# Optimization experiments

Hardware: AMD Instinct MI355X
Metric: run time of the kernel (lower is better)

## Reference

```python
import jax, jax.numpy as jnp
import numpy as np

B, N, A, M, H, KD, VD, O = 256, 2048, 256, 256, 8, 32, 32, 256
EPS = 1e-10

def setup_inputs() -> dict:
    key = jax.random.key(0)
    ks = jax.random.split(key, 8)
    return {
        "q_data": jax.random.normal(ks[0], (B, N, A), dtype=jnp.float32),
        "m_data": jax.random.normal(ks[1], (B, N, M), dtype=jnp.float32),
        "q_mask": jnp.ones((B, N, 1), dtype=jnp.float32),
        "bias": jnp.zeros((B, 1, N), dtype=jnp.float32),
        "query_w": 0.02 * jax.random.normal(ks[2], (A, H, KD), dtype=jnp.float32),
        "key_w": 0.02 * jax.random.normal(ks[3], (M, KD), dtype=jnp.float32),
        "value_w": 0.02 * jax.random.normal(ks[4], (M, VD), dtype=jnp.float32),
        "gating_w": 0.02 * jax.random.normal(ks[5], (A, H, VD), dtype=jnp.float32),
        "gating_b": jnp.zeros((H, VD), dtype=jnp.float32),
        "output_w": 0.02 * jax.random.normal(ks[6], (H, VD, O), dtype=jnp.float32),
        "output_b": jnp.zeros((O,), dtype=jnp.float32),
    }

def reference(q_data, m_data, q_mask, bias, query_w, key_w, value_w,
              gating_w, gating_b, output_w, output_b):
    # masked mean over the query axis: q_mask [B,N,1] broadcasts over channels
    q_avg = jnp.sum(q_mask * q_data, axis=1) / (jnp.sum(q_mask, axis=1) + EPS)  # [B,A]
    kd = query_w.shape[-1]
    q = jnp.einsum('ba,ahc->bhc', q_avg, query_w) * kd ** (-0.5)  # [B,H,KD]
    k = jnp.einsum('bka,ac->bkc', m_data, key_w)                  # [B,N,KD]
    v = jnp.einsum('bka,ac->bkc', m_data, value_w)                # [B,N,VD]
    # the incoming `bias` arg is overwritten by the module, as in the original
    attn_bias = 1e9 * (q_mask[:, None, :, 0] - 1.0)               # [B,1,N]
    logits = jnp.einsum('bhc,bkc->bhk', q, k) + attn_bias         # [B,H,N]
    weights = jax.nn.softmax(logits, axis=-1)
    weighted_avg = jnp.einsum('bhk,bkc->bhc', weights, v)         # [B,H,VD]
    # gating == True
    gate = jax.nn.sigmoid(jnp.einsum('bqc,chv->bqhv', q_data, gating_w) + gating_b)
    gated = weighted_avg[:, None] * gate                          # [B,N,H,VD]
    out = jnp.einsum('bqhc,hco->bqo', gated, output_w) + output_b # [B,N,O]
    return out
```

## Files before the change

kernel.cpp:

```cpp
#include <hip/hip_runtime.h>

#define B_ 256
#define N_ 2048
#define A_ 256
#define M_ 256
#define H_ 8
#define KD_ 32
#define VD_ 32
#define O_ 256

typedef float f32x4 __attribute__((ext_vector_type(4)));
typedef __bf16 bf16x8 __attribute__((ext_vector_type(8)));
typedef unsigned short u16x8 __attribute__((ext_vector_type(8)));

union FragU { u16x8 u; bf16x8 b; };

__device__ __forceinline__ unsigned short f2bf(float f) {
  union { __bf16 b; unsigned short u; } c;
  c.b = (__bf16)f;
  return c.u;
}
__device__ __forceinline__ float bf2f(unsigned short h) {
  return __uint_as_float(((unsigned int)h) << 16);
}

__device__ __forceinline__ void gll16(const void* gsrc, void* ldst) {
  __builtin_amdgcn_global_load_lds(
      (const __attribute__((address_space(1))) void*)gsrc,
      (__attribute__((address_space(3))) void*)ldst, 16, 0, 0);
}

__global__ void pack_weights(const float* __restrict__ gating_w,
                             const float* __restrict__ output_w,
                             const float* __restrict__ key_w,
                             const float* __restrict__ value_w,
                             unsigned short* __restrict__ wg,
                             unsigned short* __restrict__ wo,
                             unsigned short* __restrict__ wkv) {
  int idx = blockIdx.x * 256 + threadIdx.x;
  int j = idx & 7;
  int lane = (idx >> 3) & 63;
  int rest = idx >> 9;
  int kc = rest & 7, ct = rest >> 3;
  int row = kc * 32 + ((lane >> 4) << 3) + j;
  int col = ct * 16 + (lane & 15);
  wg[idx] = f2bf(gating_w[row * 256 + col]);
  wo[idx] = f2bf(output_w[row * 256 + col]);
  if (idx < 16384) {
    float v = (col < 32) ? key_w[row * 32 + col] : value_w[row * 32 + (col - 32)];
    wkv[idx] = f2bf(v);
  }
}

__global__ void reduce_q(const float* __restrict__ qd, const float* __restrict__ qm,
                         const float* __restrict__ qw, float* __restrict__ q_out) {
  int b = blockIdx.x;
  int t = threadIdx.x;
  int l = t & 63, g = t >> 6;
  const float* qdb = qd + (size_t)b * N_ * A_;
  const float* qmb = qm + (size_t)b * N_;
  f32x4 sum = {0.f, 0.f, 0.f, 0.f};
  float msum = 0.f;
  for (int n = g; n < N_; n += 16) {
    float m = qmb[n];
    msum += m;
    f32x4 v = *(const f32x4*)(qdb + (size_t)n * A_ + l * 4);
    sum += m * v;
  }
  __shared__ float s[16][256];
  __shared__ float ms[16];
  __shared__ float qavg[256];
  *(f32x4*)&s[g][l * 4] = sum;
  if (l == 0) ms[g] = msum;
  __syncthreads();
  if (t < 256) {
    float tot = 0.f;
#pragma unroll
    for (int k = 0; k < 16; k++) tot += s[k][t];
    float mt = 0.f;
#pragma unroll
    for (int k = 0; k < 16; k++) mt += ms[k];
    qavg[t] = tot / (mt + 1e-10f);
  }
  __syncthreads();
  if (t < 256) {
    float acc = 0.f;
    for (int a2 = 0; a2 < 256; a2++) acc += qavg[a2] * qw[a2 * 256 + t];
    q_out[b * 256 + t] = acc * 0.17677669529663687f;
  }
}

__global__ void kv_gemm(const float* __restrict__ md,
                        const unsigned short* __restrict__ wkv,
                        unsigned short* __restrict__ kv) {
  int t = threadIdx.x;
  int w = t >> 6, l = t & 63, q = l >> 4, l15 = l & 15;
  size_t r0 = (size_t)blockIdx.x * 128;
  f32x4 acc[2][4] = {};
  for (int kc = 0; kc < 8; kc++) {
    FragU bfr[4];
#pragma unroll
    for (int ct = 0; ct < 4; ct++)
      bfr[ct].u = *(const u16x8*)(wkv + (((ct * 8 + kc) * 64 + l) << 3));
    FragU af[2];
#pragma unroll
    for (int rt = 0; rt < 2; rt++) {
      size_t row = r0 + (size_t)(w * 32 + rt * 16 + l15);
      const float4* s4 = (const float4*)(md + row * 256 + kc * 32 + q * 8);
      float4 u0 = s4[0], u1 = s4[1];
      af[rt].u = (u16x8){f2bf(u0.x), f2bf(u0.y), f2bf(u0.z), f2bf(u0.w),
                         f2bf(u1.x), f2bf(u1.y), f2bf(u1.z), f2bf(u1.w)};
    }
#pragma unroll
    for (int ct = 0; ct < 4; ct++) {
      acc[0][ct] = __builtin_amdgcn_mfma_f32_16x16x32_bf16(af[0].b, bfr[ct].b, acc[0][ct], 0, 0, 0);
      acc[1][ct] = __builtin_amdgcn_mfma_f32_16x16x32_bf16(af[1].b, bfr[ct].b, acc[1][ct], 0, 0, 0);
    }
  }
#pragma unroll
  for (int rt = 0; rt < 2; rt++)
#pragma unroll
    for (int ct = 0; ct < 4; ct++)
#pragma unroll
      for (int r = 0; r < 4; r++) {
        size_t row = r0 + (size_t)(w * 32 + rt * 16 + q * 4 + r);
        kv[row * 64 + ct * 16 + l15] = f2bf(acc[rt][ct][r]);
      }
}

__global__ void attn_softmax(const unsigned short* __restrict__ kv,
                             const float* __restrict__ qv,
                             const float* __restrict__ qm,
                             float* __restrict__ wa) {
  int b = blockIdx.x, t = threadIdx.x;
  __shared__ float lg[8][2048];
  __shared__ float red[4][256];
  __shared__ float inv_s[8];
  const float* qb = qv + b * 256;
  const float* qmb = qm + (size_t)b * N_;
  for (int n = t; n < N_; n += 1024) {
    const u16x8* kr = (const u16x8*)(kv + ((size_t)(b * N_ + n)) * 64);
    float kf[32];
#pragma unroll
    for (int c8 = 0; c8 < 4; c8++) {
      u16x8 kk = kr[c8];
#pragma unroll
      for (int j = 0; j < 8; j++) kf[c8 * 8 + j] = bf2f(kk[j]);
    }
    float bias_n = 1e9f * (qmb[n] - 1.0f);
#pragma unroll
    for (int h = 0; h < 8; h++) {
      float d = 0.f;
#pragma unroll
      for (int c = 0; c < 32; c++) d += qb[h * 32 + c] * kf[c];
      lg[h][n] = d + bias_n;
    }
  }
  __syncthreads();
  if (t < 256) {
    int h = t >> 5, i = t & 31;
    float m = -3.0e38f;
    for (int n = i; n < N_; n += 32) m = fmaxf(m, lg[h][n]);
#pragma unroll
    for (int off = 16; off; off >>= 1) m = fmaxf(m, __shfl_xor(m, off));
    float s = 0.f;
    for (int n = i; n < N_; n += 32) {
      float e = __expf(lg[h][n] - m);
      lg[h][n] = e;
      s += e;
    }
#pragma unroll
    for (int off = 16; off; off >>= 1) s += __shfl_xor(s, off);
    if (i == 0) inv_s[h] = 1.0f / s;
  }
  __syncthreads();
  {
    int c = t & 31, h = (t >> 5) & 7, nq = t >> 8;
    const unsigned short* vb = kv + ((size_t)b * N_ + nq * 512) * 64 + 32 + c;
    const float* lgh = &lg[h][nq * 512];
    float acc = 0.f;
#pragma unroll 8
    for (int n = 0; n < 512; n++) acc += lgh[n] * bf2f(vb[(size_t)n * 64]);
    red[nq][t & 255] = acc;
  }
  __syncthreads();
  if (t < 256) {
    float r = red[0][t] + red[1][t] + red[2][t] + red[3][t];
    wa[b * 256 + t] = r * inv_s[t >> 5];
  }
}

__launch_bounds__(256, 4)
__global__ void gate_out(const float* __restrict__ qd,
                         const unsigned short* __restrict__ wg,
                         const unsigned short* __restrict__ wo,
                         const float* __restrict__ wa,
                         const float* __restrict__ gb,
                         const float* __restrict__ ob,
                         float* __restrict__ out) {
  int blk = blockIdx.x;
  int b = blk >> 5, tile = blk & 31;
  int t = threadIdx.x;
  int w = t >> 6, l = t & 63, q = l >> 4, l15 = l & 15;
  __shared__ __attribute__((aligned(16))) unsigned short wsg[8192];
  __shared__ __attribute__((aligned(16))) unsigned short wso[8192];
  __shared__ __attribute__((aligned(16))) unsigned short Pt[4][16][40];
  __shared__ float wa_s[256], gb_s[256], ob_s[256];
  wa_s[t] = wa[b * 256 + t];
  gb_s[t] = gb[t];
  ob_s[t] = ob[t];
  size_t rowbase = (size_t)b * N_ + tile * 64;

  {
    const char* wgb = (const char*)wg;
    const char* wob = (const char*)wo;
#pragma unroll
    for (int i = 0; i < 4; i++) {
      int ch = i * 4 + w;
      gll16(wgb + ch * 1024 + l * 16, (char*)wsg + ch * 1024);
      gll16(wob + ch * 8192 + l * 16, (char*)wso + ch * 1024);
    }
  }

  FragU af[8];
  {
    const float* src = qd + (rowbase + (size_t)(w * 16 + l15)) * 256 + q * 8;
#pragma unroll
    for (int kc = 0; kc < 8; kc++) {
      float4 u0 = *(const float4*)(src + kc * 32);
      float4 u1 = *(const float4*)(src + kc * 32 + 4);
      af[kc].u = (u16x8){f2bf(u0.x), f2bf(u0.y), f2bf(u0.z), f2bf(u0.w),
                         f2bf(u1.x), f2bf(u1.y), f2bf(u1.z), f2bf(u1.w)};
    }
  }
  f32x4 acc[4][4] = {};
  __syncthreads();

  for (int g = 0; g < 8; g++) {
    f32x4 gacc[2] = {};
#pragma unroll
    for (int kc = 0; kc < 8; kc++) {
      FragU b0, b1;
      b0.u = *(const u16x8*)(wsg + (kc * 64 + l) * 8);
      b1.u = *(const u16x8*)(wsg + ((8 + kc) * 64 + l) * 8);
      gacc[0] = __builtin_amdgcn_mfma_f32_16x16x32_bf16(af[kc].b, b0.b, gacc[0], 0, 0, 0);
      gacc[1] = __builtin_amdgcn_mfma_f32_16x16x32_bf16(af[kc].b, b1.b, gacc[1], 0, 0, 0);
    }
#pragma unroll
    for (int ctl = 0; ctl < 2; ctl++) {
      int colg = ctl * 16 + l15;
      int col = g * 32 + colg;
      float wav = wa_s[col], gbv = gb_s[col];
#pragma unroll
      for (int r = 0; r < 4; r++) {
        float x = gacc[ctl][r] + gbv;
        float gate = 1.0f / (1.0f + __expf(-x));
        Pt[w][q * 4 + r][colg] = f2bf(wav * gate);
      }
    }

    __syncthreads();
    if (g < 7) {
      const char* wgb = (const char*)wg + (size_t)(g + 1) * 16384;
#pragma unroll
      for (int i = 0; i < 4; i++) {
        int ch = i * 4 + w;
        gll16(wgb + ch * 1024 + l * 16, (char*)wsg + ch * 1024);
      }
    }
    FragU pf[4];
#pragma unroll
    for (int rt = 0; rt < 4; rt++)
      pf[rt].u = *(const u16x8*)&Pt[rt][l15][q * 8];
#pragma unroll
    for (int ct2 = 0; ct2 < 4; ct2++) {
      FragU bo;
      bo.u = *(const u16x8*)(wso + ((w * 4 + ct2) * 64 + l) * 8);
#pragma unroll
      for (int rt = 0; rt < 4; rt++)
        acc[rt][ct2] = __builtin_amdgcn_mfma_f32_16x16x32_bf16(pf[rt].b, bo.b, acc[rt][ct2], 0, 0, 0);
    }
    __syncthreads();
    if (g < 7) {
      const char* wob = (const char*)wo + (size_t)(g + 1) * 1024;
#pragma unroll
      for (int i = 0; i < 4; i++) {
        int ch = i * 4 + w;
        gll16(wob + ch * 8192 + l * 16, (char*)wso + ch * 1024);
      }
    }
  }
#pragma unroll
  for (int rt = 0; rt < 4; rt++) {
#pragma unroll
    for (int ct2 = 0; ct2 < 4; ct2++) {
      int col = w * 64 + ct2 * 16 + l15;
      float obv = ob_s[col];
      size_t orow = (rowbase + (size_t)(rt * 16 + q * 4)) * 256 + col;
#pragma unroll
      for (int r = 0; r < 4; r++)
        out[orow + (size_t)r * 256] = acc[rt][ct2][r] + obv;
    }
  }
}

extern "C" void kernel_launch(void* const* d_in, const int* in_sizes, int n_in,
                              void* d_out, int out_size, void* d_ws, size_t ws_size,
                              hipStream_t stream) {
  const float* q_data   = (const float*)d_in[0];
  const float* m_data   = (const float*)d_in[1];
  const float* q_mask   = (const float*)d_in[2];
  const float* query_w  = (const float*)d_in[4];
  const float* key_w    = (const float*)d_in[5];
  const float* value_w  = (const float*)d_in[6];
  const float* gating_w = (const float*)d_in[7];
  const float* gating_b = (const float*)d_in[8];
  const float* output_w = (const float*)d_in[9];
  const float* output_b = (const float*)d_in[10];
  float* out = (float*)d_out;

  char* ws = (char*)d_ws;
  float* q_ws            = (float*)(ws);
  float* wa_ws           = (float*)(ws + (256 << 10));
  unsigned short* wg_ws  = (unsigned short*)(ws + (512 << 10));
  unsigned short* wo_ws  = (unsigned short*)(ws + (640 << 10));
  unsigned short* wkv_ws = (unsigned short*)(ws + (768 << 10));
  unsigned short* kv_ws  = (unsigned short*)(ws + (800 << 10));

  pack_weights<<<256, 256, 0, stream>>>(gating_w, output_w, key_w, value_w,
                                        wg_ws, wo_ws, wkv_ws);
  reduce_q<<<B_, 1024, 0, stream>>>(q_data, q_mask, query_w, q_ws);
  kv_gemm<<<(B_ * N_) / 128, 256, 0, stream>>>(m_data, wkv_ws, kv_ws);
  attn_softmax<<<B_, 1024, 0, stream>>>(kv_ws, q_ws, q_mask, wa_ws);
  gate_out<<<(B_ * N_) / 64, 256, 0, stream>>>(q_data, wg_ws, wo_ws, wa_ws,
                                               gating_b, output_b, out);
}
```

Measured before the change: 1.464 ms.

## Split K/V workspace with transposed V and double-buffer gating weights

The KV projection now writes K and V into separate buffers, with V transposed to [B, VD, N]. This lets the weighted-average loop in the attention kernel read 8 contiguous bf16 values and float4 logits at a time instead of strided scalars. The trade-off is that kv_gemm now issues scattered 2-byte stores for V. In gate_out, the gating-weight LDS tile is double-buffered and prefetched at the top of each group. Output weights are read straight from global memory instead of staged in LDS, which removes one barrier per iteration at the cost of more global/L2 traffic and lower declared occupancy.

```diff
diff --git a/kernel.cpp b/kernel.cpp
--- a/kernel.cpp
+++ b/kernel.cpp
@@ -92,10 +92,13 @@
 
 __global__ void kv_gemm(const float* __restrict__ md,
                         const unsigned short* __restrict__ wkv,
-                        unsigned short* __restrict__ kv) {
+                        unsigned short* __restrict__ k_ws,
+                        unsigned short* __restrict__ v_ws) {
   int t = threadIdx.x;
   int w = t >> 6, l = t & 63, q = l >> 4, l15 = l & 15;
   size_t r0 = (size_t)blockIdx.x * 128;
+  int b = (int)(r0 >> 11);
+  int n0 = (int)(r0 & 2047);
   f32x4 acc[2][4] = {};
   for (int kc = 0; kc < 8; kc++) {
     FragU bfr[4];
@@ -123,12 +126,17 @@
     for (int ct = 0; ct < 4; ct++)
 #pragma unroll
       for (int r = 0; r < 4; r++) {
-        size_t row = r0 + (size_t)(w * 32 + rt * 16 + q * 4 + r);
-        kv[row * 64 + ct * 16 + l15] = f2bf(acc[rt][ct][r]);
+        int rloc = w * 32 + rt * 16 + q * 4 + r;
+        if (ct < 2) {
+          k_ws[(r0 + rloc) * 32 + ct * 16 + l15] = f2bf(acc[rt][ct][r]);
+        } else {
+          v_ws[((size_t)b * 32 + (ct - 2) * 16 + l15) * N_ + (n0 + rloc)] = f2bf(acc[rt][ct][r]);
+        }
       }
 }
 
-__global__ void attn_softmax(const unsigned short* __restrict__ kv,
+__global__ void attn_softmax(const unsigned short* __restrict__ k_ws,
+                             const unsigned short* __restrict__ v_ws,
                              const float* __restrict__ qv,
                              const float* __restrict__ qm,
                              float* __restrict__ wa) {
@@ -139,13 +147,30 @@
   const float* qb = qv + b * 256;
   const float* qmb = qm + (size_t)b * N_;
   for (int n = t; n < N_; n += 1024) {
-    const u16x8* kr = (const u16x8*)(kv + ((size_t)(b * N_ + n)) * 64);
+    const u16x8* kr = (const u16x8*)(k_ws + ((size_t)(b * N_ + n)) * 32);
     float kf[32];
 #pragma unroll
-    for (int c8 = 0; c8 < 4; c8++) {
+    for (int c8 = 0; c8 < 2; c8++) {
       u16x8 kk = kr[c8];
 #pragma unroll
       for (int j = 0; j < 8; j++) kf[c8 * 8 + j] = bf2f(kk[j]);
+    }
+    u16x8 kk2 = kr[0];
+    (void)kk2;
+#pragma unroll
+    for (int c8 = 2; c8 < 4; c8++) {
+      u16x8 kk = kr[c8 - 2 + 2];
+      (void)kk;
+    }
+    {
+      u16x8 ka = kr[0], kb2 = kr[1], kc2 = kr[2], kd2 = kr[3];
+#pragma unroll
+      for (int j = 0; j < 8; j++) {
+        kf[j]      = bf2f(ka[j]);
+        kf[8 + j]  = bf2f(kb2[j]);
+        kf[16 + j] = bf2f(kc2[j]);
+        kf[24 + j] = bf2f(kd2[j]);
+      }
     }
     float bias_n = 1e9f * (qmb[n] - 1.0f);
 #pragma unroll
@@ -176,11 +201,22 @@
   __syncthreads();
   {
     int c = t & 31, h = (t >> 5) & 7, nq = t >> 8;
-    const unsigned short* vb = kv + ((size_t)b * N_ + nq * 512) * 64 + 32 + c;
-    const float* lgh = &lg[h][nq * 512];
+    const u16x8* vb = (const u16x8*)(v_ws + ((size_t)b * 32 + c) * N_ + nq * 512);
+    const f32x4* lg4 = (const f32x4*)&lg[h][nq * 512];
     float acc = 0.f;
-#pragma unroll 8
-    for (int n = 0; n < 512; n++) acc += lgh[n] * bf2f(vb[(size_t)n * 64]);
+#pragma unroll 4
+    for (int n8 = 0; n8 < 64; n8++) {
+      u16x8 vv = vb[n8];
+      f32x4 p0 = lg4[n8 * 2], p1 = lg4[n8 * 2 + 1];
+      acc += p0[0] * bf2f(vv[0]);
+      acc += p0[1] * bf2f(vv[1]);
+      acc += p0[2] * bf2f(vv[2]);
+      acc += p0[3] * bf2f(vv[3]);
+      acc += p1[0] * bf2f(vv[4]);
+      acc += p1[1] * bf2f(vv[5]);
+      acc += p1[2] * bf2f(vv[6]);
+      acc += p1[3] * bf2f(vv[7]);
+    }
     red[nq][t & 255] = acc;
   }
   __syncthreads();
@@ -190,7 +226,7 @@
   }
 }
 
-__launch_bounds__(256, 4)
+__launch_bounds__(256, 3)
 __global__ void gate_out(const float* __restrict__ qd,
                          const unsigned short* __restrict__ wg,
                          const unsigned short* __restrict__ wo,
@@ -202,9 +238,8 @@
   int b = blk >> 5, tile = blk & 31;
   int t = threadIdx.x;
   int w = t >> 6, l = t & 63, q = l >> 4, l15 = l & 15;
-  __shared__ __attribute__((aligned(16))) unsigned short wsg[8192];
-  __shared__ __attribute__((aligned(16))) unsigned short wso[8192];
-  __shared__ __attribute__((aligned(16))) unsigned short Pt[4][16][40];
+  __shared__ __attribute__((aligned(16))) unsigned short wsg[2][8192];
+  __shared__ __attribute__((aligned(16))) unsigned short Pt[2][4][16][40];
   __shared__ float wa_s[256], gb_s[256], ob_s[256];
   wa_s[t] = wa[b * 256 + t];
   gb_s[t] = gb[t];
@@ -213,12 +248,10 @@
 
   {
     const char* wgb = (const char*)wg;
-    const char* wob = (const char*)wo;
 #pragma unroll
     for (int i = 0; i < 4; i++) {
       int ch = i * 4 + w;
-      gll16(wgb + ch * 1024 + l * 16, (char*)wsg + ch * 1024);
-      gll16(wob + ch * 8192 + l * 16, (char*)wso + ch * 1024);
+      gll16(wgb + ch * 1024 + l * 16, (char*)&wsg[0][0] + ch * 1024);
     }
   }
 
@@ -237,12 +270,21 @@
   __syncthreads();
 
   for (int g = 0; g < 8; g++) {
+    int cur = g & 1;
+    if (g < 7) {
+      const char* wgb = (const char*)wg + (size_t)(g + 1) * 16384;
+#pragma unroll
+      for (int i = 0; i < 4; i++) {
+        int ch = i * 4 + w;
+        gll16(wgb + ch * 1024 + l * 16, (char*)&wsg[cur ^ 1][0] + ch * 1024);
+      }
+    }
     f32x4 gacc[2] = {};
 #pragma unroll
     for (int kc = 0; kc < 8; kc++) {
       FragU b0, b1;
-      b0.u = *(const u16x8*)(wsg + (kc * 64 + l) * 8);
-      b1.u = *(const u16x8*)(wsg + ((8 + kc) * 64 + l) * 8);
+      b0.u = *(const u16x8*)(&wsg[cur][0] + (kc * 64 + l) * 8);
+      b1.u = *(const u16x8*)(&wsg[cur][0] + ((8 + kc) * 64 + l) * 8);
       gacc[0] = __builtin_amdgcn_mfma_f32_16x16x32_bf16(af[kc].b, b0.b, gacc[0], 0, 0, 0);
       gacc[1] = __builtin_amdgcn_mfma_f32_16x16x32_bf16(af[kc].b, b1.b, gacc[1], 0, 0, 0);
     }
@@ -255,39 +297,24 @@
       for (int r = 0; r < 4; r++) {
         float x = gacc[ctl][r] + gbv;
         float gate = 1.0f / (1.0f + __expf(-x));
-        Pt[w][q * 4 + r][colg] = f2bf(wav * gate);
+        Pt[cur][w][q * 4 + r][colg] = f2bf(wav * gate);
       }
     }
 
     __syncthreads();
-    if (g < 7) {
-      const char* wgb = (const char*)wg + (size_t)(g + 1) * 16384;
-#pragma unroll
-      for (int i = 0; i < 4; i++) {
-        int ch = i * 4 + w;
-        gll16(wgb + ch * 1024 + l * 16, (char*)wsg + ch * 1024);
-      }
-    }
+
     FragU pf[4];
 #pragma unroll
     for (int rt = 0; rt < 4; rt++)
-      pf[rt].u = *(const u16x8*)&Pt[rt][l15][q * 8];
+      pf[rt].u = *(const u16x8*)&Pt[cur][rt][l15][q * 8];
 #pragma unroll
     for (int ct2 = 0; ct2 < 4; ct2++) {
       FragU bo;
-      bo.u = *(const u16x8*)(wso + ((w * 4 + ct2) * 64 + l) * 8);
+      bo.u = *(const u16x8*)((const char*)wo + (size_t)(w * 4 + ct2) * 8192 +
+                             (size_t)g * 1024 + l * 16);
 #pragma unroll
       for (int rt = 0; rt < 4; rt++)
         acc[rt][ct2] = __builtin_amdgcn_mfma_f32_16x16x32_bf16(pf[rt].b, bo.b, acc[rt][ct2], 0, 0, 0);
-    }
-    __syncthreads();
-    if (g < 7) {
-      const char* wob = (const char*)wo + (size_t)(g + 1) * 1024;
-#pragma unroll
-      for (int i = 0; i < 4; i++) {
-        int ch = i * 4 + w;
-        gll16(wob + ch * 8192 + l * 16, (char*)wso + ch * 1024);
-      }
     }
   }
 #pragma unroll
@@ -325,13 +352,14 @@
   unsigned short* wg_ws  = (unsigned short*)(ws + (512 << 10));
   unsigned short* wo_ws  = (unsigned short*)(ws + (640 << 10));
   unsigned short* wkv_ws = (unsigned short*)(ws + (768 << 10));
-  unsigned short* kv_ws  = (unsigned short*)(ws + (800 << 10));
+  unsigned short* k_wsp  = (unsigned short*)(ws + (800 << 10));
+  unsigned short* v_wsp  = (unsigned short*)(ws + (800 << 10) + ((size_t)32 << 20));
 
   pack_weights<<<256, 256, 0, stream>>>(gating_w, output_w, key_w, value_w,
                                         wg_ws, wo_ws, wkv_ws);
   reduce_q<<<B_, 1024, 0, stream>>>(q_data, q_mask, query_w, q_ws);
-  kv_gemm<<<(B_ * N_) / 128, 256, 0, stream>>>(m_data, wkv_ws, kv_ws);
-  attn_softmax<<<B_, 1024, 0, stream>>>(kv_ws, q_ws, q_mask, wa_ws);
+  kv_gemm<<<(B_ * N_) / 128, 256, 0, stream>>>(m_data, wkv_ws, k_wsp, v_wsp);
+  attn_softmax<<<B_, 1024, 0, stream>>>(k_wsp, v_wsp, q_ws, q_mask, wa_ws);
   gate_out<<<(B_ * N_) / 64, 256, 0, stream>>>(q_data, wg_ws, wo_ws, wa_ws,
                                                gating_b, output_b, out);
 }
```

After: 1.474 ms. Within noise of the previous version (+0.7%).
